# Performance work log

Hardware: AMD Instinct MI355X
Metric: run time of the kernel (lower is better)

The kernel has to match this reference:

```python
import jax, jax.numpy as jnp
import numpy as np

B, S, D, H, E, K = 2, 1024, 1024, 4096, 8, 2
HE = 4 * D  # expert FFN inner dim
LN_EPS = 1e-5


def layernorm(x, g, b):
    m = x.mean(-1, keepdims=True)
    v = ((x - m) ** 2).mean(-1, keepdims=True)
    return (x - m) * jax.lax.rsqrt(v + LN_EPS) * g + b


def pos_encoding(S, D):
    pos = jnp.arange(S, dtype=jnp.float32)[:, None]
    i = jnp.arange(0, D, 2, dtype=jnp.float32)
    div = jnp.exp(-(jnp.log(10000.0)) * i / D)
    pe = jnp.zeros((S, D), dtype=jnp.float32)
    pe = pe.at[:, 0::2].set(jnp.sin(pos * div))
    pe = pe.at[:, 1::2].set(jnp.cos(pos * div))
    return pe


def setup_inputs() -> dict:
    key = jax.random.key(0)
    ks = jax.random.split(key, 16)
    w = lambda k, sh, s=0.02: (jax.random.normal(k, sh, dtype=jnp.float32) * s)
    return {
        "x": jax.random.normal(ks[0], (B, S, D), dtype=jnp.float32),
        # router: LayerNorm -> Linear(D,H) -> GELU -> Linear(H,E)
        "r_ln_g": jnp.ones((D,), jnp.float32), "r_ln_b": jnp.zeros((D,), jnp.float32),
        "r_w1": w(ks[1], (D, H)), "r_b1": jnp.zeros((H,), jnp.float32),
        "r_w2": w(ks[2], (H, E)), "r_b2": jnp.zeros((E,), jnp.float32),
        "temperature": jnp.ones((1,), jnp.float32) * 0.07,
        # stacked expert params: LayerNorm -> Linear(D,HE) -> GELU -> Linear(HE,D)
        "e_ln_g": jnp.ones((E, D), jnp.float32), "e_ln_b": jnp.zeros((E, D), jnp.float32),
        "e_w1": w(ks[3], (E, D, HE)), "e_b1": jnp.zeros((E, HE), jnp.float32),
        "e_w2": w(ks[4], (E, HE, D)), "e_b2": jnp.zeros((E, D), jnp.float32),
        # combiner: LayerNorm -> Linear(D,2D) -> GELU -> Linear(2D,D)
        "c_ln_g": jnp.ones((D,), jnp.float32), "c_ln_b": jnp.zeros((D,), jnp.float32),
        "c_w1": w(ks[5], (D, 2 * D)), "c_b1": jnp.zeros((2 * D,), jnp.float32),
        "c_w2": w(ks[6], (2 * D, D)), "c_b2": jnp.zeros((D,), jnp.float32),
        "o_ln_g": jnp.ones((D,), jnp.float32), "o_ln_b": jnp.zeros((D,), jnp.float32),
    }


def reference(x, r_ln_g, r_ln_b, r_w1, r_b1, r_w2, r_b2, temperature,
              e_ln_g, e_ln_b, e_w1, e_b1, e_w2, e_b2,
              c_ln_g, c_ln_b, c_w1, c_b1, c_w2, c_b2, o_ln_g, o_ln_b):
    gelu = lambda t: jax.nn.gelu(t, approximate=False)
    h = x + pos_encoding(S, D)[None]  # [B,S,D]
    # router logits with learned temperature
    r = layernorm(h, r_ln_g, r_ln_b)
    r = gelu(jnp.einsum("bsd,dh->bsh", r, r_w1) + r_b1)
    logits = (jnp.einsum("bsh,he->bse", r, r_w2) + r_b2) / temperature
    probs = jax.nn.softmax(logits, axis=-1)  # [B,S,E]
    topk_p, topk_i = jax.lax.top_k(probs, K)
    # sparse gate [B,S,E]: softmax prob on selected experts, 0 elsewhere
    gate = (jax.nn.one_hot(topk_i, E, dtype=probs.dtype) * topk_p[..., None]).sum(-2)
    # per-expert FFN on all tokens (dense reference of dispatch/compute/combine)
    m = h.mean(-1, keepdims=True)
    v = ((h - m) ** 2).mean(-1, keepdims=True)
    xhat = (h - m) * jax.lax.rsqrt(v + LN_EPS)  # [B,S,D], shared LN stats
    y = xhat[None] * e_ln_g[:, None, None, :] + e_ln_b[:, None, None, :]  # [E,B,S,D]
    f = gelu(jnp.einsum("ebsd,edh->ebsh", y, e_w1) + e_b1[:, None, None, :])
    f = jnp.einsum("ebsh,ehd->ebsd", f, e_w2) + e_b2[:, None, None, :]
    combined = jnp.einsum("bse,ebsd->bsd", gate, f)
    # expert combiner MLP + residual + output norm
    c = layernorm(combined, c_ln_g, c_ln_b)
    c = gelu(jnp.einsum("bsd,de->bse", c, c_w1) + c_b1)
    c = jnp.einsum("bse,ed->bsd", c, c_w2) + c_b2
    return layernorm(h + c, o_ln_g, o_ln_b)
```

## Files before the change

kernel.cpp:

```cpp
#include <hip/hip_runtime.h>
#include <stdint.h>

#define TOK 2048
#define DD  1024
#define RH  4096
#define HE  4096
#define NE  8
#define CH  2048
#define MAXTILE 40
#define MAXROWS 5120
#define KSG2 4
#define KSC1 2
#define KSC2 4

using bf16x8 = __attribute__((ext_vector_type(8))) short;
using f32x4  = __attribute__((ext_vector_type(4))) float;

__device__ __forceinline__ unsigned short f2bf(float f) {
  union { float f; uint32_t u; } v; v.f = f;
  uint32_t r = (v.u + 0x7fffu + ((v.u >> 16) & 1u)) >> 16;
  return (unsigned short)r;
}
__device__ __forceinline__ float bf2f(unsigned short h) {
  union { uint32_t u; float f; } v; v.u = ((uint32_t)h) << 16;
  return v.f;
}
__device__ __forceinline__ float gelu_f(float x) {
  return 0.5f * x * (1.0f + erff(x * 0.70710678118654752440f));
// ... 10 lines not shown
    s2 += __shfl_down(s2, off);
  }
  __shared__ float sh[8];
  int tid = threadIdx.x;
  if ((tid & 63) == 0) { sh[tid >> 6] = s1; sh[4 + (tid >> 6)] = s2; }
  __syncthreads();
  float t1 = sh[0] + sh[1] + sh[2] + sh[3];
  float t2 = sh[4] + sh[5] + sh[6] + sh[7];
  mean = t1 * (1.0f / 1024.0f);
  float var = t2 * (1.0f / 1024.0f) - mean * mean;
  rstd = rsqrtf(var + 1e-5f);
}

__global__ void k_prep(const float* __restrict__ x, float* __restrict__ h,
                       float* __restrict__ xh32, unsigned short* __restrict__ xhi,
                       unsigned short* __restrict__ xlo) {
  int t = blockIdx.x;
  int s = t & 1023;
  int tid = threadIdx.x;
  float4 xv = ((const float4*)(x + (size_t)t * DD))[tid];
  float v[4]; float s1 = 0.f, s2 = 0.f;
  #pragma unroll
  for (int k = 0; k < 4; ++k) {
    int d = tid * 4 + k;
    float xc = (k == 0) ? xv.x : (k == 1) ? xv.y : (k == 2) ? xv.z : xv.w;
    float i2 = (float)(d & ~1);
    float div = expf(-9.2103403719761836f * i2 * (1.0f / 1024.0f));
    float ang = (float)s * div;
    float pe = (d & 1) ? cosf(ang) : sinf(ang);
    float hv = xc + pe;
    v[k] = hv; s1 += hv; s2 += hv * hv;
  }
  float mean, rstd;
  block_ln_stats(s1, s2, mean, rstd);
  float4 ho; ho.x = v[0]; ho.y = v[1]; ho.z = v[2]; ho.w = v[3];
  ((float4*)(h + (size_t)t * DD))[tid] = ho;
  float xn[4]; unsigned short hh[4], ll[4];
  #pragma unroll
  for (int k = 0; k < 4; ++k) {
    xn[k] = (v[k] - mean) * rstd;
    hh[k] = f2bf(xn[k]);
    ll[k] = f2bf(xn[k] - bf2f(hh[k]));
  }
  float4 xo; xo.x = xn[0]; xo.y = xn[1]; xo.z = xn[2]; xo.w = xn[3];
  ((float4*)(xh32 + (size_t)t * DD))[tid] = xo;
  ushort4 h4; h4.x = hh[0]; h4.y = hh[1]; h4.z = hh[2]; h4.w = hh[3];
  ((ushort4*)(xhi + (size_t)t * DD))[tid] = h4;
  ushort4 l4; l4.x = ll[0]; l4.y = ll[1]; l4.z = ll[2]; l4.w = ll[3];
  ((ushort4*)(xlo + (size_t)t * DD))[tid] = l4;
}

__global__ void k_tconv(const float* __restrict__ in, const float* __restrict__ g,
                        unsigned short* __restrict__ out, int D, int N,
                        long long in_bs, long long g_bs, long long out_bs) {
  __shared__ float tile[64][65];
  int e = blockIdx.z;
  const float* inb = in + (size_t)e * in_bs;
  unsigned short* outb = out + (size_t)e * out_bs;
  int n0 = blockIdx.x * 64, d0 = blockIdx.y * 64;
  int c4 = threadIdx.x & 15;
  int r0 = threadIdx.x >> 4;
  #pragma unroll
  for (int rr = 0; rr < 4; ++rr) {
    int dl = r0 + rr * 16;
// ... 48 lines not shown
                           const float* __restrict__ b1, float* __restrict__ outb,
                           int D, int N, long long w_bs, long long lnb_bs,
                           long long b_bs, long long o_bs) {
  int e = blockIdx.y;
  int n = blockIdx.x * 256 + threadIdx.x;
  const float* wb = w + (size_t)e * w_bs;
  const float* lb = lnb + (size_t)e * lnb_bs;
  float acc = b1[(size_t)e * b_bs + n];
  for (int d = 0; d < D; ++d) {
    float l = lb[d];
    if (l != 0.f) acc += l * wb[(size_t)d * N + n];
  }
  outb[(size_t)e * o_bs + n] = acc;
}

__global__ __launch_bounds__(256)
void k_gemm_sk(const unsigned short* __restrict__ A, const unsigned short* __restrict__ B,
               float* __restrict__ C, int N, int K, int kslice, long long c_slice) {
  __shared__ __align__(16) unsigned short As[128 * 32];
  __shared__ __align__(16) unsigned short Bs[128 * 32];
  const int tid = threadIdx.x;
  const int w = tid >> 6, lane = tid & 63;
  const int q = lane >> 4, r16 = lane & 15;
  const int kz = blockIdx.z;
  const int n0 = blockIdx.x * 128, m0 = blockIdx.y * 128;
  f32x4 acc[4][4];
  #pragma unroll
  for (int i = 0; i < 4; ++i)
    #pragma unroll
    for (int j = 0; j < 4; ++j) acc[i][j] = (f32x4){0.f, 0.f, 0.f, 0.f};
  const int srow = w * 32 + (lane >> 2);
  const int scol = (lane & 3) * 8;
  const unsigned short* a_src = A + (size_t)(m0 + srow) * K + scol + (size_t)kz * kslice;
  const unsigned short* b_src = B + (size_t)(n0 + srow) * K + scol + (size_t)kz * kslice;
  unsigned short* a_dst = &As[w * 1024];
  unsigned short* b_dst = &Bs[w * 1024];
  const int wm = w >> 1, wn = w & 1;
  for (int kt = 0; kt < kslice; kt += 32) {
    GLD(a_src + kt, a_dst);
    GLD(a_src + kt + (size_t)16 * K, a_dst + 512);
    GLD(b_src + kt, b_dst);
    GLD(b_src + kt + (size_t)16 * K, b_dst + 512);
    __syncthreads();
    bf16x8 af[4], bfv[4];
    #pragma unroll
    for (int i = 0; i < 4; ++i)
      af[i] = *(const bf16x8*)&As[(wm * 64 + i * 16 + r16) * 32 + q * 8];
    #pragma unroll
    for (int j = 0; j < 4; ++j)
      bfv[j] = *(const bf16x8*)&Bs[(wn * 64 + j * 16 + r16) * 32 + q * 8];
    #pragma unroll
    for (int i = 0; i < 4; ++i)
      #pragma unroll
      for (int j = 0; j < 4; ++j)
        acc[i][j] = __builtin_amdgcn_mfma_f32_16x16x32_bf16(af[i], bfv[j], acc[i][j], 0, 0, 0);
    __syncthreads();
  }
  #pragma unroll
  for (int j = 0; j < 4; ++j) {
    int col = n0 + wn * 64 + j * 16 + r16;
    #pragma unroll
    for (int i = 0; i < 4; ++i) {
      int row = m0 + wm * 64 + i * 16 + q * 4;
      #pragma unroll
      for (int t2 = 0; t2 < 4; ++t2)
        C[(size_t)kz * c_slice + (size_t)(row + t2) * N + col] = acc[i][j][t2];
    }
  }
}

__global__ void k_redg(const float* __restrict__ p, const float* __restrict__ bias,
                       unsigned short* __restrict__ o, int N, long long slice, int nsl) {
  size_t i = ((size_t)blockIdx.x * 256 + threadIdx.x) * 4;
  float4 a = *(const float4*)(p + i);
  for (int s = 1; s < nsl; ++s) {
    float4 b = *(const float4*)(p + (size_t)s * slice + i);
    a.x += b.x; a.y += b.y; a.z += b.z; a.w += b.w;
  }
  int col = (int)(i & (size_t)(N - 1));
  float4 bv = *(const float4*)(bias + col);
  ushort4 u;
  u.x = f2bf(gelu_f(a.x + bv.x)); u.y = f2bf(gelu_f(a.y + bv.y));
  u.z = f2bf(gelu_f(a.z + bv.z)); u.w = f2bf(gelu_f(a.w + bv.w));
  *(ushort4*)(o + i) = u;
}

__global__ __launch_bounds__(256)
void k_gemm_g1(const unsigned short* __restrict__ A, const unsigned short* __restrict__ W,
               const float* __restrict__ bias, unsigned short* __restrict__ C,
               const int* __restrict__ tok_of, const int* __restrict__ tile_e,
               const int* __restrict__ tile_r0, const int* __restrict__ ntiles) {
  if ((int)blockIdx.y >= *ntiles) return;
  __shared__ __align__(16) unsigned short As[128 * 32];
  __shared__ __align__(16) unsigned short Bs[128 * 32];
  const int tid = threadIdx.x;
  const int w = tid >> 6, lane = tid & 63;
  const int q = lane >> 4, r16 = lane & 15;
  const int e = tile_e[blockIdx.y];
  const int row0 = tile_r0[blockIdx.y];
// ... 36 lines not shown
  #pragma unroll
  for (int j = 0; j < 4; ++j) {
    int col = n0 + wn * 64 + j * 16 + r16;
    float bv = bias[(size_t)e * RH + col];
    #pragma unroll
    for (int i = 0; i < 4; ++i) {
      int row = row0 + wm * 64 + i * 16 + q * 4;
      #pragma unroll
      for (int t2 = 0; t2 < 4; ++t2)
        C[(size_t)(row + t2) * RH + col] = f2bf(gelu_f(acc[i][j][t2] + bv));
    }
  }
}

__global__ __launch_bounds__(256)
void k_gemm_g2(const unsigned short* __restrict__ A, const unsigned short* __restrict__ W,
               float* __restrict__ C, const int* __restrict__ tile_e,
               const int* __restrict__ tile_r0, const int* __restrict__ ntiles) {
  if ((int)blockIdx.y >= *ntiles) return;
  __shared__ __align__(16) unsigned short As[128 * 32];
  __shared__ __align__(16) unsigned short Bs[128 * 32];
  const int tid = threadIdx.x;
  const int w = tid >> 6, lane = tid & 63;
  const int q = lane >> 4, r16 = lane & 15;
  const int e = tile_e[blockIdx.y];
  const int row0 = tile_r0[blockIdx.y];
  const int n0 = blockIdx.x * 128;
  const int kz = blockIdx.z;
  f32x4 acc[4][4];
  #pragma unroll
  for (int i = 0; i < 4; ++i)
    #pragma unroll
    for (int j = 0; j < 4; ++j) acc[i][j] = (f32x4){0.f, 0.f, 0.f, 0.f};
  const int srow = w * 32 + (lane >> 2);
  const int scol = (lane & 3) * 8;
  const unsigned short* a_src = A + (size_t)(row0 + srow) * HE + scol + (size_t)kz * (HE / KSG2);
  const unsigned short* b_src = W + (size_t)e * DD * HE + (size_t)(n0 + srow) * HE + scol
                                + (size_t)kz * (HE / KSG2);
  unsigned short* a_dst = &As[w * 1024];
  unsigned short* b_dst = &Bs[w * 1024];
  const int wm = w >> 1, wn = w & 1;
  for (int kt = 0; kt < HE / KSG2; kt += 32) {
    GLD(a_src + kt, a_dst);
    GLD(a_src + kt + (size_t)16 * HE, a_dst + 512);
    GLD(b_src + kt, b_dst);
    GLD(b_src + kt + (size_t)16 * HE, b_dst + 512);
    __syncthreads();
    bf16x8 af[4], bfv[4];
    #pragma unroll
    for (int i = 0; i < 4; ++i)
      af[i] = *(const bf16x8*)&As[(wm * 64 + i * 16 + r16) * 32 + q * 8];
    #pragma unroll
    for (int j = 0; j < 4; ++j)
      bfv[j] = *(const bf16x8*)&Bs[(wn * 64 + j * 16 + r16) * 32 + q * 8];
    #pragma unroll
    for (int i = 0; i < 4; ++i)
      #pragma unroll
      for (int j = 0; j < 4; ++j)
        acc[i][j] = __builtin_amdgcn_mfma_f32_16x16x32_bf16(af[i], bfv[j], acc[i][j], 0, 0, 0);
    __syncthreads();
  }
  #pragma unroll
  for (int j = 0; j < 4; ++j) {
    int col = n0 + wn * 64 + j * 16 + r16;
    #pragma unroll
    for (int i = 0; i < 4; ++i) {
      int row = row0 + wm * 64 + i * 16 + q * 4;
      #pragma unroll
      for (int t2 = 0; t2 < 4; ++t2)
        C[(size_t)kz * MAXROWS * DD + (size_t)(row + t2) * DD + col] = acc[i][j][t2];
    }
  }
}

__global__ __launch_bounds__(256)
void k_gemm_split(const unsigned short* __restrict__ Ah, const unsigned short* __restrict__ Al,
                  const unsigned short* __restrict__ Bh, const unsigned short* __restrict__ Bl,
                  const float* __restrict__ bias, float* __restrict__ C, int N, int K) {
  __shared__ __align__(16) unsigned short Ahs[128 * 32];
  __shared__ __align__(16) unsigned short Als[128 * 32];
  __shared__ __align__(16) unsigned short Bhs[128 * 32];
  __shared__ __align__(16) unsigned short Bls[128 * 32];
  const int tid = threadIdx.x;
  const int w = tid >> 6, lane = tid & 63;
  const int q = lane >> 4, r16 = lane & 15;
  const int n0 = blockIdx.x * 128, m0 = blockIdx.y * 128;
  f32x4 acc[4][4];
  #pragma unroll
  for (int i = 0; i < 4; ++i)
    #pragma unroll
    for (int j = 0; j < 4; ++j) acc[i][j] = (f32x4){0.f, 0.f, 0.f, 0.f};
  const int srow = w * 32 + (lane >> 2);
  const int scol = (lane & 3) * 8;
// ... 23 lines not shown
    for (int j = 0; j < 4; ++j) {
      int o = (wn * 64 + j * 16 + r16) * 32 + q * 8;
      bh[j] = *(const bf16x8*)&Bhs[o];
      bl[j] = *(const bf16x8*)&Bls[o];
    }
    #pragma unroll
    for (int i = 0; i < 4; ++i)
      #pragma unroll
      for (int j = 0; j < 4; ++j) {
        acc[i][j] = __builtin_amdgcn_mfma_f32_16x16x32_bf16(ah[i], bh[j], acc[i][j], 0, 0, 0);
        acc[i][j] = __builtin_amdgcn_mfma_f32_16x16x32_bf16(al[i], bh[j], acc[i][j], 0, 0, 0);
        acc[i][j] = __builtin_amdgcn_mfma_f32_16x16x32_bf16(ah[i], bl[j], acc[i][j], 0, 0, 0);
      }
    __syncthreads();
  }
  #pragma unroll
  for (int j = 0; j < 4; ++j) {
    int col = n0 + wn * 64 + j * 16 + r16;
    float bv = bias[col];
    #pragma unroll
    for (int i = 0; i < 4; ++i) {
      int row = m0 + wm * 64 + i * 16 + q * 4;
      #pragma unroll
      for (int t2 = 0; t2 < 4; ++t2)
        C[(size_t)(row + t2) * N + col] = gelu_f(acc[i][j][t2] + bv);
    }
  }
}

__global__ void k_logits(const float* __restrict__ r, const float* __restrict__ w2,
                         const float* __restrict__ b2, const float* __restrict__ temp,
                         int* __restrict__ sel_i, float* __restrict__ sel_p,
                         int* __restrict__ flag, float* __restrict__ lg32) {
  int t = blockIdx.x, tid = threadIdx.x;
  const float* rr = r + (size_t)t * RH;
  float acc[NE];
  #pragma unroll
  for (int e = 0; e < NE; ++e) acc[e] = 0.f;
  #pragma unroll
  for (int k4 = 0; k4 < 4; ++k4) {
    float4 rv4 = ((const float4*)rr)[tid * 4 + k4];
    #pragma unroll
    for (int kk = 0; kk < 4; ++kk) {
      int d = tid * 16 + k4 * 4 + kk;
      float rv = (kk == 0) ? rv4.x : (kk == 1) ? rv4.y : (kk == 2) ? rv4.z : rv4.w;
      const float4* wr = (const float4*)(w2 + (size_t)d * NE);
      float4 w0 = wr[0], w1 = wr[1];
      acc[0] += rv * w0.x; acc[1] += rv * w0.y; acc[2] += rv * w0.z; acc[3] += rv * w0.w;
      acc[4] += rv * w1.x; acc[5] += rv * w1.y; acc[6] += rv * w1.z; acc[7] += rv * w1.w;
    }
  }
  #pragma unroll
  for (int off = 32; off > 0; off >>= 1)
    #pragma unroll
    for (int e = 0; e < NE; ++e) acc[e] += __shfl_down(acc[e], off);
  __shared__ float shl[4][NE];
  int w = tid >> 6, lane = tid & 63;
  if (lane == 0) {
    #pragma unroll
    for (int e = 0; e < NE; ++e) shl[w][e] = acc[e];
  }
  __syncthreads();
  if (tid == 0) {
    float tmp = temp[0];
    float lg[NE];
    #pragma unroll
    for (int e = 0; e < NE; ++e)
      lg[e] = (shl[0][e] + shl[1][e] + shl[2][e] + shl[3][e] + b2[e]) / tmp;
    float mx = lg[0];
    for (int e = 1; e < NE; ++e) mx = fmaxf(mx, lg[e]);
    float p[NE], se = 0.f;
    for (int e = 0; e < NE; ++e) { p[e] = expf(lg[e] - mx); se += p[e]; }
    float inv = 1.f / se;
    int i1 = 0; float p1 = p[0];
    for (int e = 1; e < NE; ++e) if (p[e] > p1) { p1 = p[e]; i1 = e; }
    int i2 = -1; float p2 = -1.f;
    for (int e = 0; e < NE; ++e) if (e != i1 && p[e] > p2) { p2 = p[e]; i2 = e; }
    sel_i[t * 2] = i1; sel_i[t * 2 + 1] = i2;
    sel_p[t * 2] = p1 * inv; sel_p[t * 2 + 1] = p2 * inv;
    float a1 = -1e30f, a2 = -1e30f, a3 = -1e30f;
    for (int e = 0; e < NE; ++e) {
      float vv = lg[e];
      if (vv > a1) { a3 = a2; a2 = a1; a1 = vv; }
      else if (vv > a2) { a3 = a2; a2 = vv; }
      else if (vv > a3) a3 = vv;
    }
    int fl = (a2 - a3 < 0.01f) ? 1 : 0;
    flag[t] = fl;
    if (fl) {
      #pragma unroll
      for (int e = 0; e < NE; ++e) lg32[(size_t)t * NE + e] = 0.f;
    }
  }
}

__global__ void k_flaglist(const int* __restrict__ flag, int* __restrict__ ftok,
                           int* __restrict__ nflag) {
  int t = blockIdx.x * 256 + threadIdx.x;
  if (t >= TOK) return;
  if (flag[t]) { int p = atomicAdd(nflag, 1); ftok[p] = t; }
}

__global__ void k_triage2(const int* __restrict__ nflag, const int* __restrict__ ftok,
                          const float* __restrict__ xh32, const float* __restrict__ W32,
                          const float* __restrict__ biasr, const float* __restrict__ w2,
                          float* __restrict__ lg32) {
  int nf = *nflag;
  __shared__ float xs[DD];
  __shared__ float sh2[4][NE];
  int tid = threadIdx.x;
  int w = tid >> 6, lane = tid & 63;
  for (int idx = blockIdx.y; idx < nf; idx += (int)gridDim.y) {
    int t = ftok[idx];
    ((float4*)xs)[tid] = ((const float4*)(xh32 + (size_t)t * DD))[tid];
    __syncthreads();
// ... 18 lines not shown
        float r1 = gelu_f(s + biasr[hh]);
        const float* wr = w2 + (size_t)hh * NE;
        #pragma unroll
        for (int e = 0; e < NE; ++e) acc[e] += r1 * wr[e];
      }
    }
    if (lane == 0) {
      #pragma unroll
      for (int e = 0; e < NE; ++e) sh2[w][e] = acc[e];
    }
    __syncthreads();
    if (tid < NE) {
      float v = sh2[0][tid] + sh2[1][tid] + sh2[2][tid] + sh2[3][tid];
      atomicAdd(&lg32[(size_t)t * NE + tid], v);
    }
  }
}

__global__ void k_gate2(const int* __restrict__ flag, const float* __restrict__ lg32,
                        const float* __restrict__ b2, const float* __restrict__ temp,
                        int* __restrict__ sel_i, float* __restrict__ sel_p) {
  int t = blockIdx.x * 256 + threadIdx.x;
  if (t >= TOK || flag[t] == 0) return;
  float tmp = temp[0];
  float lg[NE];
  #pragma unroll
  for (int e = 0; e < NE; ++e) lg[e] = (lg32[(size_t)t * NE + e] + b2[e]) / tmp;
  float mx = lg[0];
  for (int e = 1; e < NE; ++e) mx = fmaxf(mx, lg[e]);
  float p[NE], se = 0.f;
  for (int e = 0; e < NE; ++e) { p[e] = expf(lg[e] - mx); se += p[e]; }
  float inv = 1.f / se;
  int i1 = 0; float p1 = p[0];
  for (int e = 1; e < NE; ++e) if (p[e] > p1) { p1 = p[e]; i1 = e; }
  int i2 = -1; float p2 = -1.f;
  for (int e = 0; e < NE; ++e) if (e != i1 && p[e] > p2) { p2 = p[e]; i2 = e; }
  sel_i[t * 2] = i1; sel_i[t * 2 + 1] = i2;
  sel_p[t * 2] = p1 * inv; sel_p[t * 2 + 1] = p2 * inv;
}

__global__ void k_count(const int* __restrict__ sel_i, int* __restrict__ cnt) {
  int t = blockIdx.x * 256 + threadIdx.x;
  if (t >= TOK) return;
  atomicAdd(&cnt[sel_i[2 * t]], 1);
  atomicAdd(&cnt[sel_i[2 * t + 1]], 1);
}

__global__ void k_offsets(const int* __restrict__ cnt, int* __restrict__ off,
                          int* __restrict__ tile_e, int* __restrict__ tile_r0,
                          int* __restrict__ ntiles) {
  if (threadIdx.x == 0) {
    int cur = 0, nt = 0;
    for (int e = 0; e < NE; ++e) {
      off[e] = cur;
      int n = (cnt[e] + 127) >> 7;
      for (int k = 0; k < n; ++k) { tile_e[nt] = e; tile_r0[nt] = cur + 128 * k; nt++; }
      cur += n * 128;
    }
    *ntiles = nt;
  }
// ... 3 lines not shown
                       int* __restrict__ fill, int* __restrict__ slotarr,
                       int* __restrict__ tok_of) {
  int t = blockIdx.x * 256 + threadIdx.x;
  if (t >= TOK) return;
  #pragma unroll
  for (int j = 0; j < 2; ++j) {
    int e = sel_i[2 * t + j];
    int pos = atomicAdd(&fill[e], 1);
    int s = off[e] + pos;
    slotarr[2 * t + j] = s;
    tok_of[s] = t;
  }
}

__global__ void k_combine2(const int* __restrict__ slotarr, const int* __restrict__ sel_i,
                           const float* __restrict__ sel_p, const float* __restrict__ pairpart,
                           const float* __restrict__ e_b2, unsigned short* __restrict__ xc) {
  int t = blockIdx.x, tid = threadIdx.x;
  int s0 = slotarr[t * 2], s1 = slotarr[t * 2 + 1];
  int e0 = sel_i[t * 2], e1 = sel_i[t * 2 + 1];
  float w0 = sel_p[t * 2], w1 = sel_p[t * 2 + 1];
  float a0x = 0.f, a0y = 0.f, a0z = 0.f, a0w = 0.f;
  float a1x = 0.f, a1y = 0.f, a1z = 0.f, a1w = 0.f;
  #pragma unroll
  for (int z = 0; z < KSG2; ++z) {
    float4 u = ((const float4*)(pairpart + (size_t)z * MAXROWS * DD + (size_t)s0 * DD))[tid];
    a0x += u.x; a0y += u.y; a0z += u.z; a0w += u.w;
    float4 v = ((const float4*)(pairpart + (size_t)z * MAXROWS * DD + (size_t)s1 * DD))[tid];
    a1x += v.x; a1y += v.y; a1z += v.z; a1w += v.w;
  }
  float4 b0 = ((const float4*)(e_b2 + (size_t)e0 * DD))[tid];
  float4 b1v = ((const float4*)(e_b2 + (size_t)e1 * DD))[tid];
  float v[4];
  v[0] = w0 * (a0x + b0.x) + w1 * (a1x + b1v.x);
  v[1] = w0 * (a0y + b0.y) + w1 * (a1y + b1v.y);
  v[2] = w0 * (a0z + b0.z) + w1 * (a1z + b1v.z);
  v[3] = w0 * (a0w + b0.w) + w1 * (a1w + b1v.w);
  float s1f = v[0] + v[1] + v[2] + v[3];
  float s2f = v[0]*v[0] + v[1]*v[1] + v[2]*v[2] + v[3]*v[3];
  float mean, rstd;
  block_ln_stats(s1f, s2f, mean, rstd);
  ushort4 o;
  o.x = f2bf((v[0] - mean) * rstd); o.y = f2bf((v[1] - mean) * rstd);
  o.z = f2bf((v[2] - mean) * rstd); o.w = f2bf((v[3] - mean) * rstd);
  ((ushort4*)(xc + (size_t)t * DD))[tid] = o;
}

__global__ void k_final(const float* __restrict__ h, const float* __restrict__ c2p,
                        const float* __restrict__ cb2, const float* __restrict__ og,
                        const float* __restrict__ ob, float* __restrict__ out) {
  int t = blockIdx.x, tid = threadIdx.x;
  float4 hv = ((const float4*)(h + (size_t)t * DD))[tid];
// ... 47 lines not shown
  const float* o_ln_b = (const float*)d_in[21];
  float* out = (float*)d_out;

  char* base = (char*)d_ws;
  long long cur = 0;
  auto take = [&](long long sz) { char* r = base + cur; cur += (sz + 255) & ~255LL; return r; };

  float* h      = (float*)take(8388608);
  float* xh32   = (float*)take(8388608);
  unsigned short* xhi = (unsigned short*)take(4194304);
  unsigned short* xlo = (unsigned short*)take(4194304);
  unsigned short* WrH = (unsigned short*)take(8388608);
  unsigned short* WrL = (unsigned short*)take(8388608);
  float* Wr32   = (float*)take(16777216);
  float* biasr  = (float*)take(16384);
  float* ract   = (float*)take(33554432);
  int*   flag   = (int*)take(8192);
  float* lg32   = (float*)take(65536);
  int*   sel_i  = (int*)take(16384);
  float* sel_p  = (float*)take(16384);
  int*   cnt    = (int*)take(256);
  int*   off    = (int*)take(256);
  int*   fillc  = (int*)take(256);
  int*   tile_e = (int*)take(256);
  int*   tile_r0= (int*)take(256);
  int*   ntiles = (int*)take(256);
  int*   nflag  = (int*)take(256);
  int*   ftok   = (int*)take(TOK * 4);
  int*   slotarr= (int*)take(16384);
  int*   tok_of = (int*)take(MAXROWS * 4);
  unsigned short* We1 = (unsigned short*)take(67108864);
  float* be1    = (float*)take(131072);
  unsigned short* We2 = (unsigned short*)take(67108864);
  unsigned short* Wc1 = (unsigned short*)take(4194304);
  float* bc1    = (float*)take(8192);
  unsigned short* Wc2 = (unsigned short*)take(4194304);
  unsigned short* xc  = (unsigned short*)take(4194304);
  unsigned short* c1  = (unsigned short*)take(8388608);
  unsigned short* F1g = (unsigned short*)take((long long)MAXROWS * RH * 2);
  float* pairpart = (float*)take((long long)KSG2 * MAXROWS * DD * 4);
  float* c1part = (float*)WrH;
  float* c2part = (float*)biasr;

  hipMemsetAsync(cnt, 0, 256, stream);
  hipMemsetAsync(fillc, 0, 256, stream);
  hipMemsetAsync(nflag, 0, 256, stream);
  hipMemsetAsync(tok_of, 0, MAXROWS * 4, stream);

  k_prep<<<TOK, 256, 0, stream>>>(x, h, xh32, xhi, xlo);
  k_tconv_split<<<dim3(RH/32, DD/32, 1), 256, 0, stream>>>(r_w1, r_ln_g, WrH, WrL, Wr32, DD, RH);
  k_tconv<<<dim3(RH/64, DD/64, NE), 256, 0, stream>>>(e_w1, e_ln_g, We1, DD, RH,
      (long long)DD*RH, (long long)DD, (long long)RH*DD);
  k_tconv<<<dim3(DD/64, HE/64, NE), 256, 0, stream>>>(e_w2, nullptr, We2, HE, DD,
      (long long)HE*DD, 0LL, (long long)DD*HE);
  k_tconv<<<dim3(CH/64, DD/64, 1), 256, 0, stream>>>(c_w1, c_ln_g, Wc1, DD, CH, 0LL, 0LL, 0LL);
  k_tconv<<<dim3(DD/64, CH/64, 1), 256, 0, stream>>>(c_w2, nullptr, Wc2, CH, DD, 0LL, 0LL, 0LL);
  k_foldbias<<<dim3(RH/256, 1), 256, 0, stream>>>(r_w1, r_ln_b, r_b1, biasr, DD, RH, 0LL, 0LL, 0LL, 0LL);
  k_foldbias<<<dim3(RH/256, NE), 256, 0, stream>>>(e_w1, e_ln_b, e_b1, be1, DD, RH,
      (long long)DD*RH, (long long)DD, (long long)RH, (long long)RH);
  k_foldbias<<<dim3(CH/256, 1), 256, 0, stream>>>(c_w1, c_ln_b, c_b1, bc1, DD, CH, 0LL, 0LL, 0LL, 0LL);

  k_gemm_split<<<dim3(RH/128, TOK/128, 1), 256, 0, stream>>>(xhi, xlo, WrH, WrL, biasr, ract, RH, DD);
  k_logits<<<TOK, 256, 0, stream>>>(ract, r_w2, r_b2, temp, sel_i, sel_p, flag, lg32);
  k_flaglist<<<TOK/256, 256, 0, stream>>>(flag, ftok, nflag);
  k_triage2<<<dim3(RH/64, 32), 256, 0, stream>>>(nflag, ftok, xh32, Wr32, biasr, r_w2, lg32);
  k_gate2<<<TOK/256, 256, 0, stream>>>(flag, lg32, r_b2, temp, sel_i, sel_p);

  k_count<<<TOK/256, 256, 0, stream>>>(sel_i, cnt);
  k_offsets<<<1, 64, 0, stream>>>(cnt, off, tile_e, tile_r0, ntiles);
  k_fill<<<TOK/256, 256, 0, stream>>>(sel_i, off, fillc, slotarr, tok_of);

  k_gemm_g1<<<dim3(RH/128, MAXTILE), 256, 0, stream>>>(xhi, We1, be1, F1g,
      tok_of, tile_e, tile_r0, ntiles);
  k_gemm_g2<<<dim3(DD/128, MAXTILE, KSG2), 256, 0, stream>>>(F1g, We2, pairpart,
      tile_e, tile_r0, ntiles);

  k_combine2<<<TOK, 256, 0, stream>>>(slotarr, sel_i, sel_p, pairpart, e_b2, xc);
  k_gemm_sk<<<dim3(CH/128, TOK/128, KSC1), 256, 0, stream>>>(xc, Wc1, c1part, CH, DD,
      DD/KSC1, (long long)TOK * CH);
  k_redg<<<(TOK * CH) / 1024, 256, 0, stream>>>(c1part, bc1, c1, CH, (long long)TOK * CH, KSC1);
  k_gemm_sk<<<dim3(DD/128, TOK/128, KSC2), 256, 0, stream>>>(c1, Wc2, c2part, DD, CH,
      CH/KSC2, (long long)TOK * DD);
  k_final<<<TOK, 256, 0, stream>>>(h, c2part, c_b2, o_ln_g, o_ln_b, out);
}
```

Baseline: 1.097 ms.

## Fuse router logits into split GEMM, drop split-K reductions, merge small kernels

Computes router logits inside the router GEMM epilogue as per-column-tile partial sums, so the fp32 router activation buffer is never written. A gate kernel reduces those partials, and the flag-list and count steps are merged into the gate kernels. Expert GEMM2 and combiner GEMM1 switch to 64-wide N tiles without split-K, writing bf16 outputs with bias and GELU fused in the epilogue. This removes the partial-sum traffic and the separate reduction kernel. Memsets move into the prep kernel, and positional encoding uses sincosf. The price is bf16 rounding of expert outputs and a longer K loop per block.

Result: faster. 1.050 ms (-4.3%).

```diff
diff --git a/kernel.cpp b/kernel.cpp
--- a/kernel.cpp
+++ b/kernel.cpp
@@ -9,9 +9,7 @@
 #define CH  2048
 #define MAXTILE 40
 #define MAXROWS 5120
-#define KSG2 4
-#define KSC1 2
-#define KSC2 4
+#define KSC2 2
 
 using bf16x8 = __attribute__((ext_vector_type(8))) short;
 using f32x4  = __attribute__((ext_vector_type(4))) float;
@@ -52,23 +50,27 @@
 
 __global__ void k_prep(const float* __restrict__ x, float* __restrict__ h,
                        float* __restrict__ xh32, unsigned short* __restrict__ xhi,
-                       unsigned short* __restrict__ xlo) {
+                       unsigned short* __restrict__ xlo, int* __restrict__ cnt,
+                       int* __restrict__ fillc, int* __restrict__ nflag,
+                       int* __restrict__ tok_of) {
   int t = blockIdx.x;
   int s = t & 1023;
   int tid = threadIdx.x;
   float4 xv = ((const float4*)(x + (size_t)t * DD))[tid];
   float v[4]; float s1 = 0.f, s2 = 0.f;
   #pragma unroll
-  for (int k = 0; k < 4; ++k) {
-    int d = tid * 4 + k;
-    float xc = (k == 0) ? xv.x : (k == 1) ? xv.y : (k == 2) ? xv.z : xv.w;
-    float i2 = (float)(d & ~1);
+  for (int kp = 0; kp < 2; ++kp) {
+    float i2 = (float)(tid * 4 + kp * 2);
     float div = expf(-9.2103403719761836f * i2 * (1.0f / 1024.0f));
     float ang = (float)s * div;
-    float pe = (d & 1) ? cosf(ang) : sinf(ang);
-    float hv = xc + pe;
-    v[k] = hv; s1 += hv; s2 += hv * hv;
-  }
+    float sn, cs;
+    sincosf(ang, &sn, &cs);
+    float xe = (kp == 0) ? xv.x : xv.z;
+    float xo = (kp == 0) ? xv.y : xv.w;
+    v[kp * 2] = xe + sn; v[kp * 2 + 1] = xo + cs;
+  }
+  #pragma unroll
+  for (int k = 0; k < 4; ++k) { s1 += v[k]; s2 += v[k] * v[k]; }
   float mean, rstd;
   block_ln_stats(s1, s2, mean, rstd);
   float4 ho; ho.x = v[0]; ho.y = v[1]; ho.z = v[2]; ho.w = v[3];
@@ -80,12 +82,17 @@
     hh[k] = f2bf(xn[k]);
     ll[k] = f2bf(xn[k] - bf2f(hh[k]));
   }
-  float4 xo; xo.x = xn[0]; xo.y = xn[1]; xo.z = xn[2]; xo.w = xn[3];
-  ((float4*)(xh32 + (size_t)t * DD))[tid] = xo;
+  float4 xo4; xo4.x = xn[0]; xo4.y = xn[1]; xo4.z = xn[2]; xo4.w = xn[3];
+  ((float4*)(xh32 + (size_t)t * DD))[tid] = xo4;
   ushort4 h4; h4.x = hh[0]; h4.y = hh[1]; h4.z = hh[2]; h4.w = hh[3];
   ((ushort4*)(xhi + (size_t)t * DD))[tid] = h4;
   ushort4 l4; l4.x = ll[0]; l4.y = ll[1]; l4.z = ll[2]; l4.w = ll[3];
   ((ushort4*)(xlo + (size_t)t * DD))[tid] = l4;
+  if (t == 0) {
+    for (int i = tid; i < MAXROWS; i += 256) tok_of[i] = 0;
+    if (tid < NE) { cnt[tid] = 0; fillc[tid] = 0; }
+    if (tid == 0) nflag[0] = 0;
+  }
 }
 
 __global__ void k_tconv(const float* __restrict__ in, const float* __restrict__ g,
@@ -164,75 +171,69 @@
   outb[(size_t)e * o_bs + n] = acc;
 }
 
+template <int DO_GELU, int OUT_BF16>
 __global__ __launch_bounds__(256)
-void k_gemm_sk(const unsigned short* __restrict__ A, const unsigned short* __restrict__ B,
-               float* __restrict__ C, int N, int K, int kslice, long long c_slice) {
+void k_gemm_n64(const unsigned short* __restrict__ A, const unsigned short* __restrict__ B,
+                const float* __restrict__ bias, void* __restrict__ Cv, int N, int K,
+                int kslice, long long c_slice) {
   __shared__ __align__(16) unsigned short As[128 * 32];
-  __shared__ __align__(16) unsigned short Bs[128 * 32];
+  __shared__ __align__(16) unsigned short Bs[64 * 32];
   const int tid = threadIdx.x;
   const int w = tid >> 6, lane = tid & 63;
   const int q = lane >> 4, r16 = lane & 15;
   const int kz = blockIdx.z;
-  const int n0 = blockIdx.x * 128, m0 = blockIdx.y * 128;
-  f32x4 acc[4][4];
+  const int n0 = blockIdx.x * 64, m0 = blockIdx.y * 128;
+  f32x4 acc[4][2];
   #pragma unroll
   for (int i = 0; i < 4; ++i)
     #pragma unroll
-    for (int j = 0; j < 4; ++j) acc[i][j] = (f32x4){0.f, 0.f, 0.f, 0.f};
+    for (int j = 0; j < 2; ++j) acc[i][j] = (f32x4){0.f, 0.f, 0.f, 0.f};
   const int srow = w * 32 + (lane >> 2);
+  const int bsrow = (w < 2) ? srow : 0;
   const int scol = (lane & 3) * 8;
   const unsigned short* a_src = A + (size_t)(m0 + srow) * K + scol + (size_t)kz * kslice;
-  const unsigned short* b_src = B + (size_t)(n0 + srow) * K + scol + (size_t)kz * kslice;
+  const unsigned short* b_src = B + (size_t)(n0 + bsrow) * K + scol + (size_t)kz * kslice;
   unsigned short* a_dst = &As[w * 1024];
-  unsigned short* b_dst = &Bs[w * 1024];
+  unsigned short* b_dst = &Bs[(w & 1) * 1024];
   const int wm = w >> 1, wn = w & 1;
   for (int kt = 0; kt < kslice; kt += 32) {
     GLD(a_src + kt, a_dst);
     GLD(a_src + kt + (size_t)16 * K, a_dst + 512);
-    GLD(b_src + kt, b_dst);
-    GLD(b_src + kt + (size_t)16 * K, b_dst + 512);
-    __syncthreads();
-    bf16x8 af[4], bfv[4];
+    if (w < 2) {
+      GLD(b_src + kt, b_dst);
+      GLD(b_src + kt + (size_t)16 * K, b_dst + 512);
+    }
+    __syncthreads();
+    bf16x8 af[4], bfv[2];
     #pragma unroll
     for (int i = 0; i < 4; ++i)
       af[i] = *(const bf16x8*)&As[(wm * 64 + i * 16 + r16) * 32 + q * 8];
     #pragma unroll
-    for (int j = 0; j < 4; ++j)
-      bfv[j] = *(const bf16x8*)&Bs[(wn * 64 + j * 16 + r16) * 32 + q * 8];
+    for (int j = 0; j < 2; ++j)
+      bfv[j] = *(const bf16x8*)&Bs[(wn * 32 + j * 16 + r16) * 32 + q * 8];
     #pragma unroll
     for (int i = 0; i < 4; ++i)
       #pragma unroll
-      for (int j = 0; j < 4; ++j)
+      for (int j = 0; j < 2; ++j)
         acc[i][j] = __builtin_amdgcn_mfma_f32_16x16x32_bf16(af[i], bfv[j], acc[i][j], 0, 0, 0);
     __syncthreads();
   }
   #pragma unroll
-  for (int j = 0; j < 4; ++j) {
-    int col = n0 + wn * 64 + j * 16 + r16;
+  for (int j = 0; j < 2; ++j) {
+    int col = n0 + wn * 32 + j * 16 + r16;
+    float bv = bias ? bias[col] : 0.f;
     #pragma unroll
     for (int i = 0; i < 4; ++i) {
       int row = m0 + wm * 64 + i * 16 + q * 4;
       #pragma unroll
-      for (int t2 = 0; t2 < 4; ++t2)
-        C[(size_t)kz * c_slice + (size_t)(row + t2) * N + col] = acc[i][j][t2];
-    }
-  }
-}
-
-__global__ void k_redg(const float* __restrict__ p, const float* __restrict__ bias,
-                       unsigned short* __restrict__ o, int N, long long slice, int nsl) {
-  size_t i = ((size_t)blockIdx.x * 256 + threadIdx.x) * 4;
-  float4 a = *(const float4*)(p + i);
-  for (int s = 1; s < nsl; ++s) {
-    float4 b = *(const float4*)(p + (size_t)s * slice + i);
-    a.x += b.x; a.y += b.y; a.z += b.z; a.w += b.w;
-  }
-  int col = (int)(i & (size_t)(N - 1));
-  float4 bv = *(const float4*)(bias + col);
-  ushort4 u;
-  u.x = f2bf(gelu_f(a.x + bv.x)); u.y = f2bf(gelu_f(a.y + bv.y));
-  u.z = f2bf(gelu_f(a.z + bv.z)); u.w = f2bf(gelu_f(a.w + bv.w));
-  *(ushort4*)(o + i) = u;
+      for (int t2 = 0; t2 < 4; ++t2) {
+        float vv = acc[i][j][t2] + bv;
+        if (DO_GELU) vv = gelu_f(vv);
+        if (OUT_BF16) ((unsigned short*)Cv)[(size_t)(row + t2) * N + col] = f2bf(vv);
+        else ((float*)Cv)[(size_t)kz * c_slice + (size_t)(row + t2) * N + col] = vv;
+      }
+    }
+  }
 }
 
 __global__ __launch_bounds__(256)
@@ -299,61 +300,62 @@
 }
 
 __global__ __launch_bounds__(256)
-void k_gemm_g2(const unsigned short* __restrict__ A, const unsigned short* __restrict__ W,
-               float* __restrict__ C, const int* __restrict__ tile_e,
-               const int* __restrict__ tile_r0, const int* __restrict__ ntiles) {
+void k_gemm_g2n(const unsigned short* __restrict__ A, const unsigned short* __restrict__ W,
+                unsigned short* __restrict__ C, const int* __restrict__ tile_e,
+                const int* __restrict__ tile_r0, const int* __restrict__ ntiles) {
   if ((int)blockIdx.y >= *ntiles) return;
   __shared__ __align__(16) unsigned short As[128 * 32];
-  __shared__ __align__(16) unsigned short Bs[128 * 32];
+  __shared__ __align__(16) unsigned short Bs[64 * 32];
   const int tid = threadIdx.x;
   const int w = tid >> 6, lane = tid & 63;
   const int q = lane >> 4, r16 = lane & 15;
   const int e = tile_e[blockIdx.y];
   const int row0 = tile_r0[blockIdx.y];
-  const int n0 = blockIdx.x * 128;
-  const int kz = blockIdx.z;
-  f32x4 acc[4][4];
+  const int n0 = blockIdx.x * 64;
+  f32x4 acc[4][2];
   #pragma unroll
   for (int i = 0; i < 4; ++i)
     #pragma unroll
-    for (int j = 0; j < 4; ++j) acc[i][j] = (f32x4){0.f, 0.f, 0.f, 0.f};
+    for (int j = 0; j < 2; ++j) acc[i][j] = (f32x4){0.f, 0.f, 0.f, 0.f};
   const int srow = w * 32 + (lane >> 2);
+  const int bsrow = (w < 2) ? srow : 0;
   const int scol = (lane & 3) * 8;
-  const unsigned short* a_src = A + (size_t)(row0 + srow) * HE + scol + (size_t)kz * (HE / KSG2);
-  const unsigned short* b_src = W + (size_t)e * DD * HE + (size_t)(n0 + srow) * HE + scol
-                                + (size_t)kz * (HE / KSG2);
+  const unsigned short* a_src = A + (size_t)(row0 + srow) * HE + scol;
+  const unsigned short* b_src = W + (size_t)e * DD * HE + (size_t)(n0 + bsrow) * HE + scol;
   unsigned short* a_dst = &As[w * 1024];
-  unsigned short* b_dst = &Bs[w * 1024];
+  unsigned short* b_dst = &Bs[(w & 1) * 1024];
   const int wm = w >> 1, wn = w & 1;
-  for (int kt = 0; kt < HE / KSG2; kt += 32) {
+  for (int kt = 0; kt < HE; kt += 32) {
     GLD(a_src + kt, a_dst);
     GLD(a_src + kt + (size_t)16 * HE, a_dst + 512);
-    GLD(b_src + kt, b_dst);
-    GLD(b_src + kt + (size_t)16 * HE, b_dst + 512);
-    __syncthreads();
-    bf16x8 af[4], bfv[4];
+    if (w < 2) {
+      GLD(b_src + kt, b_dst);
+      GLD(b_src + kt + (size_t)16 * HE, b_dst + 512);
+    }
+    __syncthreads();
+    bf16x8 af[4], bfv[2];
     #pragma unroll
     for (int i = 0; i < 4; ++i)
       af[i] = *(const bf16x8*)&As[(wm * 64 + i * 16 + r16) * 32 + q * 8];
     #pragma unroll
-    for (int j = 0; j < 4; ++j)
-      bfv[j] = *(const bf16x8*)&Bs[(wn * 64 + j * 16 + r16) * 32 + q * 8];
+    for (int j = 0; j < 2; ++j)
+      bfv[j] = *(const bf16x8*)&Bs[(wn * 32 + j * 16 + r16) * 32 + q * 8];
     #pragma unroll
     for (int i = 0; i < 4; ++i)
       #pragma unroll
-      for (int j = 0; j < 4; ++j)
+      for (int j = 0; j < 2; ++j)
         acc[i][j] = __builtin_amdgcn_mfma_f32_16x16x32_bf16(af[i], bfv[j], acc[i][j], 0, 0, 0);
     __syncthreads();
   }
   #pragma unroll
-  for (int j = 0; j < 4; ++j) {
-    int col = n0 + wn * 64 + j * 16 + r16;
+  for (int j = 0; j < 2; ++j) {
+    int col = n0 + wn * 32 + j * 16 + r16;
     #pragma unroll
     for (int i = 0; i < 4; ++i) {
       int row = row0 + wm * 64 + i * 16 + q * 4;
       #pragma unroll
       for (int t2 = 0; t2 < 4; ++t2)
-        C[(size_t)kz * MAXROWS * DD + (size_t)(row + t2) * DD + col] = acc[i][j][t2];
+        C[(size_t)(row + t2) * DD + col] = f2bf(acc[i][j][t2]);
     }
   }
 }
@@ -361,7 +363,8 @@
 __global__ __launch_bounds__(256)
 void k_gemm_split(const unsigned short* __restrict__ Ah, const unsigned short* __restrict__ Al,
                   const unsigned short* __restrict__ Bh, const unsigned short* __restrict__ Bl,
-                  const float* __restrict__ bias, float* __restrict__ C, int N, int K) {
+                  const float* __restrict__ bias, const float* __restrict__ w2,
+                  float* __restrict__ lgp, int K) {
   __shared__ __align__(16) unsigned short Ahs[128 * 32];
   __shared__ __align__(16) unsigned short Als[128 * 32];
   __shared__ __align__(16) unsigned short Bhs[128 * 32];
@@ -415,91 +418,94 @@
       }
     __syncthreads();
   }
+  float w2v[4][8], bv[4];
   #pragma unroll
   for (int j = 0; j < 4; ++j) {
     int col = n0 + wn * 64 + j * 16 + r16;
-    float bv = bias[col];
-    #pragma unroll
-    for (int i = 0; i < 4; ++i) {
-      int row = m0 + wm * 64 + i * 16 + q * 4;
-      #pragma unroll
-      for (int t2 = 0; t2 < 4; ++t2)
-        C[(size_t)(row + t2) * N + col] = gelu_f(acc[i][j][t2] + bv);
-    }
-  }
-}
-
-__global__ void k_logits(const float* __restrict__ r, const float* __restrict__ w2,
-                         const float* __restrict__ b2, const float* __restrict__ temp,
-                         int* __restrict__ sel_i, float* __restrict__ sel_p,
-                         int* __restrict__ flag, float* __restrict__ lg32) {
-  int t = blockIdx.x, tid = threadIdx.x;
-  const float* rr = r + (size_t)t * RH;
-  float acc[NE];
-  #pragma unroll
-  for (int e = 0; e < NE; ++e) acc[e] = 0.f;
-  #pragma unroll
-  for (int k4 = 0; k4 < 4; ++k4) {
-    float4 rv4 = ((const float4*)rr)[tid * 4 + k4];
-    #pragma unroll
-    for (int kk = 0; kk < 4; ++kk) {
-      int d = tid * 16 + k4 * 4 + kk;
-      float rv = (kk == 0) ? rv4.x : (kk == 1) ? rv4.y : (kk == 2) ? rv4.z : rv4.w;
-      const float4* wr = (const float4*)(w2 + (size_t)d * NE);
-      float4 w0 = wr[0], w1 = wr[1];
-      acc[0] += rv * w0.x; acc[1] += rv * w0.y; acc[2] += rv * w0.z; acc[3] += rv * w0.w;
-      acc[4] += rv * w1.x; acc[5] += rv * w1.y; acc[6] += rv * w1.z; acc[7] += rv * w1.w;
-    }
-  }
-  #pragma unroll
-  for (int off = 32; off > 0; off >>= 1)
-    #pragma unroll
-    for (int e = 0; e < NE; ++e) acc[e] += __shfl_down(acc[e], off);
-  __shared__ float shl[4][NE];
-  int w = tid >> 6, lane = tid & 63;
-  if (lane == 0) {
-    #pragma unroll
-    for (int e = 0; e < NE; ++e) shl[w][e] = acc[e];
-  }
+    bv[j] = bias[col];
+    const float4* wr = (const float4*)(w2 + (size_t)col * 8);
+    float4 u = wr[0], v2 = wr[1];
+    w2v[j][0] = u.x;  w2v[j][1] = u.y;  w2v[j][2] = u.z;  w2v[j][3] = u.w;
+    w2v[j][4] = v2.x; w2v[j][5] = v2.y; w2v[j][6] = v2.z; w2v[j][7] = v2.w;
+  }
+  float* plog = (float*)Ahs;
+  #pragma unroll
+  for (int idx = 0; idx < 4; ++idx) plog[idx * 256 + tid] = 0.f;
   __syncthreads();
-  if (tid == 0) {
-    float tmp = temp[0];
-    float lg[NE];
-    #pragma unroll
-    for (int e = 0; e < NE; ++e)
-      lg[e] = (shl[0][e] + shl[1][e] + shl[2][e] + shl[3][e] + b2[e]) / tmp;
-    float mx = lg[0];
-    for (int e = 1; e < NE; ++e) mx = fmaxf(mx, lg[e]);
-    float p[NE], se = 0.f;
-    for (int e = 0; e < NE; ++e) { p[e] = expf(lg[e] - mx); se += p[e]; }
-    float inv = 1.f / se;
-    int i1 = 0; float p1 = p[0];
-    for (int e = 1; e < NE; ++e) if (p[e] > p1) { p1 = p[e]; i1 = e; }
-    int i2 = -1; float p2 = -1.f;
-    for (int e = 0; e < NE; ++e) if (e != i1 && p[e] > p2) { p2 = p[e]; i2 = e; }
-    sel_i[t * 2] = i1; sel_i[t * 2 + 1] = i2;
-    sel_p[t * 2] = p1 * inv; sel_p[t * 2 + 1] = p2 * inv;
-    float a1 = -1e30f, a2 = -1e30f, a3 = -1e30f;
-    for (int e = 0; e < NE; ++e) {
-      float vv = lg[e];
-      if (vv > a1) { a3 = a2; a2 = a1; a1 = vv; }
-      else if (vv > a2) { a3 = a2; a2 = vv; }
-      else if (vv > a3) a3 = vv;
-    }
-    int fl = (a2 - a3 < 0.01f) ? 1 : 0;
-    flag[t] = fl;
-    if (fl) {
-      #pragma unroll
-      for (int e = 0; e < NE; ++e) lg32[(size_t)t * NE + e] = 0.f;
-    }
-  }
-}
-
-__global__ void k_flaglist(const int* __restrict__ flag, int* __restrict__ ftok,
-                           int* __restrict__ nflag) {
+  #pragma unroll
+  for (int i = 0; i < 4; ++i)
+    #pragma unroll
+    for (int t2 = 0; t2 < 4; ++t2) {
+      int rloc = wm * 64 + i * 16 + q * 4 + t2;
+      float a8[8];
+      #pragma unroll
+      for (int e2 = 0; e2 < 8; ++e2) a8[e2] = 0.f;
+      #pragma unroll
+      for (int j = 0; j < 4; ++j) {
+        float v = gelu_f(acc[i][j][t2] + bv[j]);
+        #pragma unroll
+        for (int e2 = 0; e2 < 8; ++e2) a8[e2] += v * w2v[j][e2];
+      }
+      #pragma unroll
+      for (int off = 8; off > 0; off >>= 1)
+        #pragma unroll
+        for (int e2 = 0; e2 < 8; ++e2) a8[e2] += __shfl_down(a8[e2], off, 16);
+      if (r16 == 0) {
+        #pragma unroll
+        for (int e2 = 0; e2 < 8; ++e2) atomicAdd(&plog[rloc * 8 + e2], a8[e2]);
+      }
+    }
+  __syncthreads();
+  float4* dst = (float4*)(lgp + ((size_t)blockIdx.x * TOK + m0) * 8);
+  dst[tid] = ((float4*)plog)[tid];
+}
+
+__global__ void k_gate1(const float* __restrict__ lgp, const float* __restrict__ b2,
+                        const float* __restrict__ temp, int* __restrict__ sel_i,
+                        float* __restrict__ sel_p, int* __restrict__ flag,
+                        float* __restrict__ lg32, int* __restrict__ nflag,
+                        int* __restrict__ ftok) {
   int t = blockIdx.x * 256 + threadIdx.x;
   if (t >= TOK) return;
-  if (flag[t]) { int p = atomicAdd(nflag, 1); ftok[p] = t; }
+  float s8[NE];
+  #pragma unroll
+  for (int e = 0; e < NE; ++e) s8[e] = 0.f;
+  for (int c = 0; c < RH / 128; ++c) {
+    const float4* p = (const float4*)(lgp + ((size_t)c * TOK + t) * 8);
+    float4 u = p[0], v = p[1];
+    s8[0] += u.x; s8[1] += u.y; s8[2] += u.z; s8[3] += u.w;
+    s8[4] += v.x; s8[5] += v.y; s8[6] += v.z; s8[7] += v.w;
+  }
+  float tmp = temp[0];
+  float lg[NE];
+  #pragma unroll
+  for (int e = 0; e < NE; ++e) lg[e] = (s8[e] + b2[e]) / tmp;
+  float mx = lg[0];
+  for (int e = 1; e < NE; ++e) mx = fmaxf(mx, lg[e]);
+  float p[NE], se = 0.f;
+  for (int e = 0; e < NE; ++e) { p[e] = expf(lg[e] - mx); se += p[e]; }
+  float inv = 1.f / se;
+  int i1 = 0; float p1 = p[0];
+  for (int e = 1; e < NE; ++e) if (p[e] > p1) { p1 = p[e]; i1 = e; }
+  int i2 = -1; float p2 = -1.f;
+  for (int e = 0; e < NE; ++e) if (e != i1 && p[e] > p2) { p2 = p[e]; i2 = e; }
+  sel_i[t * 2] = i1; sel_i[t * 2 + 1] = i2;
+  sel_p[t * 2] = p1 * inv; sel_p[t * 2 + 1] = p2 * inv;
+  float a1 = -1e30f, a2 = -1e30f, a3 = -1e30f;
+  for (int e = 0; e < NE; ++e) {
+    float vv = lg[e];
+    if (vv > a1) { a3 = a2; a2 = a1; a1 = vv; }
+    else if (vv > a2) { a3 = a2; a2 = vv; }
+    else if (vv > a3) a3 = vv;
+  }
+  int fl = (a2 - a3 < 0.01f) ? 1 : 0;
+  flag[t] = fl;
+  if (fl) {
+    int pidx = atomicAdd(nflag, 1);
+    ftok[pidx] = t;
+    #pragma unroll
+    for (int e = 0; e < NE; ++e) lg32[(size_t)t * NE + e] = 0.f;
+  }
 }
 
 __global__ void k_triage2(const int* __restrict__ nflag, const int* __restrict__ ftok,
@@ -548,36 +554,38 @@
       float v = sh2[0][tid] + sh2[1][tid] + sh2[2][tid] + sh2[3][tid];
       atomicAdd(&lg32[(size_t)t * NE + tid], v);
     }
+    __syncthreads();
   }
 }
 
 __global__ void k_gate2(const int* __restrict__ flag, const float* __restrict__ lg32,
                         const float* __restrict__ b2, const float* __restrict__ temp,
-                        int* __restrict__ sel_i, float* __restrict__ sel_p) {
-  int t = blockIdx.x * 256 + threadIdx.x;
-  if (t >= TOK || flag[t] == 0) return;
-  float tmp = temp[0];
-  float lg[NE];
-  #pragma unroll
-  for (int e = 0; e < NE; ++e) lg[e] = (lg32[(size_t)t * NE + e] + b2[e]) / tmp;
-  float mx = lg[0];
-  for (int e = 1; e < NE; ++e) mx = fmaxf(mx, lg[e]);
-  float p[NE], se = 0.f;
-  for (int e = 0; e < NE; ++e) { p[e] = expf(lg[e] - mx); se += p[e]; }
-  float inv = 1.f / se;
-  int i1 = 0; float p1 = p[0];
-  for (int e = 1; e < NE; ++e) if (p[e] > p1) { p1 = p[e]; i1 = e; }
-  int i2 = -1; float p2 = -1.f;
-  for (int e = 0; e < NE; ++e) if (e != i1 && p[e] > p2) { p2 = p[e]; i2 = e; }
-  sel_i[t * 2] = i1; sel_i[t * 2 + 1] = i2;
-  sel_p[t * 2] = p1 * inv; sel_p[t * 2 + 1] = p2 * inv;
-}
-
-__global__ void k_count(const int* __restrict__ sel_i, int* __restrict__ cnt) {
+                        int* __restrict__ sel_i, float* __restrict__ sel_p,
+                        int* __restrict__ cnt) {
   int t = blockIdx.x * 256 + threadIdx.x;
   if (t >= TOK) return;
-  atomicAdd(&cnt[sel_i[2 * t]], 1);
-  atomicAdd(&cnt[sel_i[2 * t + 1]], 1);
+  int i1, i2;
+  if (flag[t]) {
+    float tmp = temp[0];
+    float lg[NE];
+    #pragma unroll
+    for (int e = 0; e < NE; ++e) lg[e] = (lg32[(size_t)t * NE + e] + b2[e]) / tmp;
+    float mx = lg[0];
+    for (int e = 1; e < NE; ++e) mx = fmaxf(mx, lg[e]);
+    float p[NE], se = 0.f;
+    for (int e = 0; e < NE; ++e) { p[e] = expf(lg[e] - mx); se += p[e]; }
+    float inv = 1.f / se;
+    i1 = 0; float p1 = p[0];
+    for (int e = 1; e < NE; ++e) if (p[e] > p1) { p1 = p[e]; i1 = e; }
+    i2 = -1; float p2 = -1.f;
+    for (int e = 0; e < NE; ++e) if (e != i1 && p[e] > p2) { p2 = p[e]; i2 = e; }
+    sel_i[t * 2] = i1; sel_i[t * 2 + 1] = i2;
+    sel_p[t * 2] = p1 * inv; sel_p[t * 2 + 1] = p2 * inv;
+  } else {
+    i1 = sel_i[t * 2]; i2 = sel_i[t * 2 + 1];
+  }
+  atomicAdd(&cnt[i1], 1);
+  atomicAdd(&cnt[i2], 1);
 }
 
 __global__ void k_offsets(const int* __restrict__ cnt, int* __restrict__ off,
@@ -611,28 +619,21 @@
 }
 
 __global__ void k_combine2(const int* __restrict__ slotarr, const int* __restrict__ sel_i,
-                           const float* __restrict__ sel_p, const float* __restrict__ pairpart,
+                           const float* __restrict__ sel_p, const unsigned short* __restrict__ pairout,
                            const float* __restrict__ e_b2, unsigned short* __restrict__ xc) {
   int t = blockIdx.x, tid = threadIdx.x;
   int s0 = slotarr[t * 2], s1 = slotarr[t * 2 + 1];
   int e0 = sel_i[t * 2], e1 = sel_i[t * 2 + 1];
   float w0 = sel_p[t * 2], w1 = sel_p[t * 2 + 1];
-  float a0x = 0.f, a0y = 0.f, a0z = 0.f, a0w = 0.f;
-  float a1x = 0.f, a1y = 0.f, a1z = 0.f, a1w = 0.f;
-  #pragma unroll
-  for (int z = 0; z < KSG2; ++z) {
-    float4 u = ((const float4*)(pairpart + (size_t)z * MAXROWS * DD + (size_t)s0 * DD))[tid];
-    a0x += u.x; a0y += u.y; a0z += u.z; a0w += u.w;
-    float4 v = ((const float4*)(pairpart + (size_t)z * MAXROWS * DD + (size_t)s1 * DD))[tid];
-    a1x += v.x; a1y += v.y; a1z += v.z; a1w += v.w;
-  }
+  ushort4 u0 = ((const ushort4*)(pairout + (size_t)s0 * DD))[tid];
+  ushort4 u1 = ((const ushort4*)(pairout + (size_t)s1 * DD))[tid];
   float4 b0 = ((const float4*)(e_b2 + (size_t)e0 * DD))[tid];
   float4 b1v = ((const float4*)(e_b2 + (size_t)e1 * DD))[tid];
   float v[4];
-  v[0] = w0 * (a0x + b0.x) + w1 * (a1x + b1v.x);
-  v[1] = w0 * (a0y + b0.y) + w1 * (a1y + b1v.y);
-  v[2] = w0 * (a0z + b0.z) + w1 * (a1z + b1v.z);
-  v[3] = w0 * (a0w + b0.w) + w1 * (a1w + b1v.w);
+  v[0] = w0 * (bf2f(u0.x) + b0.x) + w1 * (bf2f(u1.x) + b1v.x);
+  v[1] = w0 * (bf2f(u0.y) + b0.y) + w1 * (bf2f(u1.y) + b1v.y);
+  v[2] = w0 * (bf2f(u0.z) + b0.z) + w1 * (bf2f(u1.z) + b1v.z);
+  v[3] = w0 * (bf2f(u0.w) + b0.w) + w1 * (bf2f(u1.w) + b1v.w);
   float s1f = v[0] + v[1] + v[2] + v[3];
   float s2f = v[0]*v[0] + v[1]*v[1] + v[2]*v[2] + v[3]*v[3];
   float mean, rstd;
@@ -710,7 +711,7 @@
   unsigned short* WrL = (unsigned short*)take(8388608);
   float* Wr32   = (float*)take(16777216);
   float* biasr  = (float*)take(16384);
-  float* ract   = (float*)take(33554432);
+  float* lgp    = (float*)take((long long)(RH/128) * TOK * NE * 4);
   int*   flag   = (int*)take(8192);
   float* lg32   = (float*)take(65536);
   int*   sel_i  = (int*)take(16384);
@@ -734,16 +735,10 @@
   unsigned short* xc  = (unsigned short*)take(4194304);
   unsigned short* c1  = (unsigned short*)take(8388608);
   unsigned short* F1g = (unsigned short*)take((long long)MAXROWS * RH * 2);
-  float* pairpart = (float*)take((long long)KSG2 * MAXROWS * DD * 4);
-  float* c1part = (float*)WrH;
-  float* c2part = (float*)biasr;
-
-  hipMemsetAsync(cnt, 0, 256, stream);
-  hipMemsetAsync(fillc, 0, 256, stream);
-  hipMemsetAsync(nflag, 0, 256, stream);
-  hipMemsetAsync(tok_of, 0, MAXROWS * 4, stream);
-
-  k_prep<<<TOK, 256, 0, stream>>>(x, h, xh32, xhi, xlo);
+  unsigned short* pairout = (unsigned short*)take((long long)MAXROWS * DD * 2);
+  float* c2part = (float*)take((long long)KSC2 * TOK * DD * 4);
+
+  k_prep<<<TOK, 256, 0, stream>>>(x, h, xh32, xhi, xlo, cnt, fillc, nflag, tok_of);
   k_tconv_split<<<dim3(RH/32, DD/32, 1), 256, 0, stream>>>(r_w1, r_ln_g, WrH, WrL, Wr32, DD, RH);
   k_tconv<<<dim3(RH/64, DD/64, NE), 256, 0, stream>>>(e_w1, e_ln_g, We1, DD, RH,
       (long long)DD*RH, (long long)DD, (long long)RH*DD);
@@ -756,26 +751,24 @@
       (long long)DD*RH, (long long)DD, (long long)RH, (long long)RH);
   k_foldbias<<<dim3(CH/256, 1), 256, 0, stream>>>(c_w1, c_ln_b, c_b1, bc1, DD, CH, 0LL, 0LL, 0LL, 0LL);
 
-  k_gemm_split<<<dim3(RH/128, TOK/128, 1), 256, 0, stream>>>(xhi, xlo, WrH, WrL, biasr, ract, RH, DD);
-  k_logits<<<TOK, 256, 0, stream>>>(ract, r_w2, r_b2, temp, sel_i, sel_p, flag, lg32);
-  k_flaglist<<<TOK/256, 256, 0, stream>>>(flag, ftok, nflag);
+  k_gemm_split<<<dim3(RH/128, TOK/128, 1), 256, 0, stream>>>(xhi, xlo, WrH, WrL, biasr,
+      r_w2, lgp, DD);
+  k_gate1<<<TOK/256, 256, 0, stream>>>(lgp, r_b2, temp, sel_i, sel_p, flag, lg32, nflag, ftok);
   k_triage2<<<dim3(RH/64, 32), 256, 0, stream>>>(nflag, ftok, xh32, Wr32, biasr, r_w2, lg32);
-  k_gate2<<<TOK/256, 256, 0, stream>>>(flag, lg32, r_b2, temp, sel_i, sel_p);
-
-  k_count<<<TOK/256, 256, 0, stream>>>(sel_i, cnt);
+  k_gate2<<<TOK/256, 256, 0, stream>>>(flag, lg32, r_b2, temp, sel_i, sel_p, cnt);
+
   k_offsets<<<1, 64, 0, stream>>>(cnt, off, tile_e, tile_r0, ntiles);
   k_fill<<<TOK/256, 256, 0, stream>>>(sel_i, off, fillc, slotarr, tok_of);
 
   k_gemm_g1<<<dim3(RH/128, MAXTILE), 256, 0, stream>>>(xhi, We1, be1, F1g,
       tok_of, tile_e, tile_r0, ntiles);
-  k_gemm_g2<<<dim3(DD/128, MAXTILE, KSG2), 256, 0, stream>>>(F1g, We2, pairpart,
+  k_gemm_g2n<<<dim3(DD/64, MAXTILE), 256, 0, stream>>>(F1g, We2, pairout,
       tile_e, tile_r0, ntiles);
 
-  k_combine2<<<TOK, 256, 0, stream>>>(slotarr, sel_i, sel_p, pairpart, e_b2, xc);
-  k_gemm_sk<<<dim3(CH/128, TOK/128, KSC1), 256, 0, stream>>>(xc, Wc1, c1part, CH, DD,
-      DD/KSC1, (long long)TOK * CH);
-  k_redg<<<(TOK * CH) / 1024, 256, 0, stream>>>(c1part, bc1, c1, CH, (long long)TOK * CH, KSC1);
-  k_gemm_sk<<<dim3(DD/128, TOK/128, KSC2), 256, 0, stream>>>(c1, Wc2, c2part, DD, CH,
-      CH/KSC2, (long long)TOK * DD);
+  k_combine2<<<TOK, 256, 0, stream>>>(slotarr, sel_i, sel_p, pairout, e_b2, xc);
+  k_gemm_n64<1,1><<<dim3(CH/64, TOK/128, 1), 256, 0, stream>>>(xc, Wc1, bc1, (void*)c1,
+      CH, DD, DD, 0LL);
+  k_gemm_n64<0,0><<<dim3(DD/64, TOK/128, KSC2), 256, 0, stream>>>(c1, Wc2, nullptr,
+      (void*)c2part, DD, CH, CH/KSC2, (long long)TOK * DD);
   k_final<<<TOK, 256, 0, stream>>>(h, c2part, c_b2, o_ln_g, o_ln_b, out);
 }
```
